# Optimization experiments

Hardware: AMD Instinct MI355X
Metric: run time of the kernel (lower is better)

## Reference

```python
import jax, jax.numpy as jnp
import numpy as np

N = 50000        # nodes
E = 600000       # edges (avg degree 12)
NODE, EDGE, GDIM = 15, 10, 8
HID, L, H = 128, 3, 4
D = HID // H     # per-head dim = 32


def setup_inputs() -> dict:
    key = jax.random.key(0)
    ks = jax.random.split(key, 32)
    f = lambda i, shape, s=0.05: jax.random.normal(ks[i], shape, dtype=jnp.float32) * s
    return {
        "x": f(0, (N, NODE), 1.0),
        "edge_index": jax.random.randint(ks[1], (2, E), 0, N, dtype=jnp.int32),
        "edge_attr": f(2, (E, EDGE), 1.0),
        "u": f(3, (GDIM,), 1.0),
        "enc_w": f(4, (NODE, HID)), "enc_b": f(5, (HID,)),
        "gat_lin_w": f(6, (L, HID, HID)),
        "gat_att_src": f(7, (L, H, D)), "gat_att_dst": f(8, (L, H, D)),
        "gat_lin_edge": f(9, (L, EDGE, HID)), "gat_att_edge": f(10, (L, H, D)),
        "gat_bias": f(11, (L, HID)),
        "ln_g": jnp.ones((L, HID), jnp.float32), "ln_b": jnp.zeros((L, HID), jnp.float32),
        "pool_w": f(12, (3 * HID + GDIM, GDIM)), "pool_b": f(13, (GDIM,)),
        "pool_ln_g": jnp.ones((GDIM,), jnp.float32), "pool_ln_b": jnp.zeros((GDIM,), jnp.float32),
        "head_w1": f(14, (4, HID, 32)), "head_b1": f(15, (4, 32)),
        "head_w2": f(16, (4, 32, 1)), "head_b2": f(17, (4, 1)),
        "strat_w1": f(18, (HID, 32)), "strat_b1": f(19, (32,)),
        "strat_w2": f(20, (32, 5)), "strat_b2": f(21, (5,)),
        "glob_w1": f(22, (GDIM, 32)), "glob_b1": f(23, (32,)),
        "glob_w2": f(24, (32, 4)), "glob_b2": f(25, (4,)),
    }


def _layer_norm(x, g, b, eps=1e-5):
    mu = jnp.mean(x, axis=-1, keepdims=True)
    var = jnp.mean(jnp.square(x - mu), axis=-1, keepdims=True)
    return (x - mu) * jax.lax.rsqrt(var + eps) * g + b


def _forward(edge_index, x, edge_attr, u, enc_w, enc_b, gat_lin_w, gat_att_src,
             gat_att_dst, gat_lin_edge, gat_att_edge, gat_bias, ln_g, ln_b,
             pool_w, pool_b, pool_ln_g, pool_ln_b, head_w1, head_b1, head_w2,
             head_b2, strat_w1, strat_b1, strat_w2, strat_b2, glob_w1, glob_b1,
             glob_w2, glob_b2):
    src0, dst0 = edge_index[0], edge_index[1]
    # PyG GATConv add_self_loops=True with fill_value='mean': self-loop edge
    # attr for node i = mean of edge_attr over edges whose dst is i.
    cnt = jax.ops.segment_sum(jnp.ones((E,), jnp.float32), dst0, num_segments=N)
    ea_self = jax.ops.segment_sum(edge_attr, dst0, num_segments=N) / jnp.maximum(cnt, 1.0)[:, None]
    loop = jnp.arange(N, dtype=src0.dtype)
    src = jnp.concatenate([src0, loop])
    dst = jnp.concatenate([dst0, loop])
    ea = jnp.concatenate([edge_attr, ea_self], axis=0)   # [E+N, EDGE]

    h = jax.nn.relu(x @ enc_w + enc_b)                   # node encoder [N, HID]
    for l in range(L):
        hp = (h @ gat_lin_w[l]).reshape(N, H, D)         # projected nodes
        a_s = jnp.sum(hp * gat_att_src[l], axis=-1)      # [N, H]
        a_d = jnp.sum(hp * gat_att_dst[l], axis=-1)
        ep = (ea @ gat_lin_edge[l]).reshape(-1, H, D)    # [E+N, H, D]
        a_e = jnp.sum(ep * gat_att_edge[l], axis=-1)     # [E+N, H]
        alpha = jax.nn.leaky_relu(a_s[src] + a_d[dst] + a_e, negative_slope=0.2)
        # numerically-stable softmax over incoming edges per dst node
        m = jax.ops.segment_max(alpha, dst, num_segments=N)
        w = jnp.exp(alpha - m[dst])
        denom = jax.ops.segment_sum(w, dst, num_segments=N)
        attn = w / denom[dst]                            # every node has a self-loop
        out = jax.ops.segment_sum(hp[src] * attn[..., None], dst, num_segments=N)
        out = out.reshape(N, HID) + gat_bias[l]
        # residual (shapes match) + dropout(eval=id) + layer norm
        h = _layer_norm(h + out, ln_g[l], ln_b[l])

    pooled = jnp.concatenate([h.mean(0), h.max(0), h.sum(0), u])[None]  # [1, 3*HID+GDIM]
    g = _layer_norm(jax.nn.relu(pooled @ pool_w + pool_b), pool_ln_g, pool_ln_b)

    # four stacked 128->32->1 heads (priority:tanh, coop/urgency/safety:sigmoid)
    z = jax.nn.relu(jnp.einsum('nf,kfh->knh', h, head_w1) + head_b1[:, None, :])
    y = jnp.einsum('knh,kho->kno', z, head_w2) + head_b2[:, None, :]   # [4, N, 1]
    priority = jnp.tanh(y[0])
    cooperation = jax.nn.sigmoid(y[1])
    urgency = jax.nn.sigmoid(y[2])
    safety = jax.nn.sigmoid(y[3])
    strategies = jax.nn.softmax(jax.nn.relu(h @ strat_w1 + strat_b1) @ strat_w2 + strat_b2, axis=-1)
    global_signal = jnp.tanh(jax.nn.relu(g @ glob_w1 + glob_b1) @ glob_w2 + glob_b2)[0]  # [4]
    return (priority, cooperation, urgency, safety, strategies, global_signal)


def reference(x, edge_index, edge_attr, u, enc_w, enc_b, gat_lin_w, gat_att_src,
              gat_att_dst, gat_lin_edge, gat_att_edge, gat_bias, ln_g, ln_b,
              pool_w, pool_b, pool_ln_g, pool_ln_b, head_w1, head_b1, head_w2,
              head_b2, strat_w1, strat_b1, strat_w2, strat_b2, glob_w1, glob_b1,
              glob_w2, glob_b2):
    return _forward(edge_index, x, edge_attr, u, enc_w, enc_b, gat_lin_w,
                    gat_att_src, gat_att_dst, gat_lin_edge, gat_att_edge,
                    gat_bias, ln_g, ln_b, pool_w, pool_b, pool_ln_g, pool_ln_b,
                    head_w1, head_b1, head_w2, head_b2, strat_w1, strat_b1,
                    strat_w2, strat_b2, glob_w1, glob_b1, glob_w2, glob_b2)
```

## Files before the change

kernel.cpp:

```cpp
#include <hip/hip_runtime.h>
#include <hip/hip_bf16.h>
#include <hip/hip_fp16.h>

#define N_NODES 50000
#define N_EDGES 600000
#define TOT_E   (N_EDGES + N_NODES)
#define NLAYER  3
#define PB      200
#define SCB     512
#define NSB     ((N_NODES + SCB - 1)/SCB)
#define CAP     96

typedef __hip_bfloat16 bf16;
__device__ __forceinline__ float b2f(bf16 v){ return __bfloat162float(v); }

__device__ __forceinline__ float ldm(const void* p, long i, int m){
  return m ? ((const float*)p)[i] : b2f(((const bf16*)p)[i]);
}

__global__ void detect_kernel(const void* probe, int* mode){
  __shared__ float red[256];
  int t = threadIdx.x;
  const bf16* p = (const bf16*)probe;
  float mx = 0.f;
  for (int i = t; i < 1920; i += 256){
    float v = fabsf(b2f(p[i]));
    if (!isfinite(v)) v = 1e30f;
    mx = fmaxf(mx, v);
  }
  red[t] = mx; __syncthreads();
  if (t == 0){
    float m = 0.f;
    for (int i = 0; i < 256; i++) m = fmaxf(m, red[i]);
    mode[0] = (m > 1000.0f) ? 1 : 0;
  }
}

__global__ void sentinel_kernel(int host_code, const int* devflags, const int* mode, float* out){
  if (threadIdx.x == 0 && blockIdx.x == 0){
    int code = host_code;
    if (!code && devflags){
      if (devflags[1] > 900)      code = 16384;
      else if (devflags[0])       code = 20480;
    }
    if (code){
      if (mode) code += 512*mode[0];
      out[0] = (float)code;
    }
  }
}

struct CvtTab { const void* s[27]; float* d[27]; int n[27]; };
__global__ void cvt_small_kernel(CvtTab tab, const int* mode){
  int b = blockIdx.x;
  int i = blockIdx.y*256 + threadIdx.x;
  if (i < tab.n[b]) tab.d[b][i] = ldm(tab.s[b], i, mode[0]);
}

__global__ void count_kernel(const int* __restrict__ ei, int* __restrict__ cnt, int* devflags){
  int e = blockIdx.x*256 + threadIdx.x;
  if (e >= N_EDGES) return;
  int s = ei[e], d = ei[N_EDGES + e];
  if (((unsigned)s >= N_NODES) || ((unsigned)d >= N_NODES)) atomicOr(&devflags[0], 1);
  else atomicAdd(&cnt[d], 1);
  if (e < 1024 && ei[2*e + 1] == 0) atomicAdd(&devflags[1], 1);
}

__global__ __launch_bounds__(SCB) void scan1_kernel(const int* __restrict__ cnt, int* __restrict__ bsum){
  __shared__ int ws[SCB/64];
  int i = blockIdx.x*SCB + threadIdx.x;
  int v = (i < N_NODES) ? cnt[i] + 1 : 0;
  int lane = threadIdx.x & 63, w = threadIdx.x >> 6;
  #pragma unroll
  for (int off = 1; off < 64; off <<= 1) v += __shfl_xor(v, off);
  if (lane == 0) ws[w] = v;
  __syncthreads();
  if (threadIdx.x == 0){
    int s = 0;
    #pragma unroll
    for (int k = 0; k < SCB/64; k++) s += ws[k];
    bsum[blockIdx.x] = s;
  }
}

__global__ void scan2_kernel(int* __restrict__ bsum, int* __restrict__ rowptr){
  if (threadIdx.x == 0 && blockIdx.x == 0){
    int run = 0;
    for (int b = 0; b < NSB; b++){ int t = bsum[b]; bsum[b] = run; run += t; }
    rowptr[N_NODES] = run;
  }
}

__global__ __launch_bounds__(SCB) void scan3_kernel(const int* __restrict__ cnt, const int* __restrict__ bsum,
                                                    int* __restrict__ rowptr){
  __shared__ int sm[SCB];
  int t = threadIdx.x;
  int i = blockIdx.x*SCB + t;
  int v = (i < N_NODES) ? cnt[i] + 1 : 0;
  sm[t] = v; __syncthreads();
  for (int off = 1; off < SCB; off <<= 1){
    int add = (t >= off) ? sm[t-off] : 0;
    __syncthreads();
    sm[t] += add;
    __syncthreads();
  }
  if (i < N_NODES) rowptr[i] = bsum[blockIdx.x] + sm[t] - v;
}

__global__ void scatter_kernel(const int* __restrict__ ei, const int* __restrict__ rowptr,
                               int* __restrict__ fill, int* __restrict__ srcs, int* __restrict__ pos_of){
  int e = blockIdx.x*256 + threadIdx.x;
  if (e >= TOT_E) return;
  if (e < N_EDGES){
    int s = ei[e], d = ei[N_EDGES + e];
    int pos = rowptr[d] + atomicAdd(&fill[d], 1);
    srcs[pos] = s; pos_of[e] = pos;
  } else {
    int i = e - N_EDGES;
    srcs[rowptr[i+1] - 1] = i;
  }
}

__global__ void pack_kernel(const float* __restrict__ head_w1, const float* __restrict__ strat_w1,
                            const float* __restrict__ head_b1, const float* __restrict__ strat_b1,
                            float* __restrict__ W1cat, float* __restrict__ b1cat){
  int t = blockIdx.x*256 + threadIdx.x;
  if (t < 128*160){
    int f = t / 160, c = t % 160;
    W1cat[t] = (c < 128) ? head_w1[(c>>5)*4096 + f*32 + (c&31)]
                         : strat_w1[f*32 + (c-128)];
  }
  if (t < 160) b1cat[t] = (t < 128) ? head_b1[t] : strat_b1[t-128];
}

__global__ void mmat_kernel(const float* __restrict__ We, const float* __restrict__ att_edge,
                            float* __restrict__ M){
  int t = threadIdx.x;
  if (t >= 120) return;
  int l = t / 40, r = t % 40, k = r / 4, hh = r % 4;
  float s = 0;
  #pragma unroll
  for (int d = 0; d < 32; d++)
    s += We[l*1280 + k*128 + hh*32 + d] * att_edge[l*128 + hh*32 + d];
  M[t] = s;
}

__global__ __launch_bounds__(128) void encoder_kernel(const void* __restrict__ x_raw, const int* __restrict__ mode,
                                                      const float* __restrict__ enc_w, const float* __restrict__ enc_b,
                                                      float* __restrict__ h){
  __shared__ float xs[16];
  int n = blockIdx.x, j = threadIdx.x;
  if (j < 15) xs[j] = ldm(x_raw, (long)n*15 + j, mode[0]);
  __syncthreads();
  float acc = enc_b[j];
  #pragma unroll
  for (int k = 0; k < 15; k++) acc += xs[k] * enc_w[k*128 + j];
  h[(size_t)n*128 + j] = fmaxf(acc, 0.0f);
}

__global__ void ae_kernel(const void* __restrict__ ea_raw, const int* __restrict__ mode,
                          const float* __restrict__ Mmat, const int* __restrict__ pos_of,
                          float4* __restrict__ aec){
  int e = blockIdx.x*256 + threadIdx.x;
  if (e >= N_EDGES) return;
  int m = mode[0];
  float v[10];
  #pragma unroll
  for (int k = 0; k < 10; k++) v[k] = ldm(ea_raw, (long)e*10 + k, m);
  int p = pos_of[e];
  #pragma unroll
  for (int l = 0; l < 3; l++){
    float r[4];
    #pragma unroll
    for (int hh = 0; hh < 4; hh++){
      float s = 0;
      #pragma unroll
      for (int k = 0; k < 10; k++) s += v[k]*Mmat[l*40 + k*4 + hh];
      r[hh] = s;
    }
    aec[(size_t)l*TOT_E + p] = make_float4(r[0], r[1], r[2], r[3]);
  }
}

#define BK 16
__global__ __launch_bounds__(256) void gemm_kernel(
    const float* __restrict__ A, const float* __restrict__ B, float* __restrict__ Cf,
    __half* __restrict__ Ch, int M, int ldb, int mode, const float* __restrict__ bias,
    const float* __restrict__ att_src, const float* __restrict__ att_dst,
    float* __restrict__ a_s, float* __restrict__ a_d){
  __shared__ float As[BK][128+4];
  __shared__ float Bs[BK][128];
  int t = threadIdx.x;
  int tx = t & 15, ty = t >> 4;
  int n0 = blockIdx.x * 128;
  int j0 = blockIdx.y * 128;
  float acc[8][8];
  #pragma unroll
  for (int i = 0; i < 8; i++)
    #pragma unroll
    for (int j = 0; j < 8; j++) acc[i][j] = 0.0f;

  for (int kb = 0; kb < 128; kb += BK){
    #pragma unroll
    for (int q = 0; q < 2; q++){
      int v = t*2 + q;
      int row = v >> 2, c4 = v & 3;
      int gn = n0 + row;
      float4 f = make_float4(0,0,0,0);
      if (gn < M) f = *(const float4*)(A + (size_t)gn*128 + kb + c4*4);
      As[c4*4+0][row] = f.x; As[c4*4+1][row] = f.y;
      As[c4*4+2][row] = f.z; As[c4*4+3][row] = f.w;
    }
    #pragma unroll
    for (int q = 0; q < 2; q++){
      int v = t*2 + q;
      int kk = v >> 5, j4 = v & 31;
      int gj = j0 + j4*4;
      float4 f = make_float4(0,0,0,0);
      if (gj < ldb) f = *(const float4*)(B + (size_t)(kb+kk)*ldb + gj);
      *(float4*)&Bs[kk][j4*4] = f;
    }
    __syncthreads();
    #pragma unroll
    for (int kk = 0; kk < BK; kk++){
      float4 a0 = *(const float4*)&As[kk][ty*8];
      float4 a1 = *(const float4*)&As[kk][ty*8+4];
      float4 b0 = *(const float4*)&Bs[kk][tx*8];
      float4 b1 = *(const float4*)&Bs[kk][tx*8+4];
      float av[8] = {a0.x,a0.y,a0.z,a0.w,a1.x,a1.y,a1.z,a1.w};
      float bv[8] = {b0.x,b0.y,b0.z,b0.w,b1.x,b1.y,b1.z,b1.w};
      #pragma unroll
      for (int i = 0; i < 8; i++)
        #pragma unroll
        for (int j = 0; j < 8; j++) acc[i][j] += av[i]*bv[j];
    }
    __syncthreads();
  }

  if (mode == 0){
    int head = tx >> 2;
    float as_w[8], ad_w[8];
    #pragma unroll
    for (int jj = 0; jj < 8; jj++){
      int dd = (tx&3)*8 + jj;
      as_w[jj] = att_src[head*32 + dd];
      ad_w[jj] = att_dst[head*32 + dd];
    }
    #pragma unroll
    for (int i = 0; i < 8; i++){
      int gn = n0 + ty*8 + i;
      float ps = 0, pd = 0;
      #pragma unroll
      for (int jj = 0; jj < 8; jj++){ ps += acc[i][jj]*as_w[jj]; pd += acc[i][jj]*ad_w[jj]; }
      ps += __shfl_xor(ps, 1); ps += __shfl_xor(ps, 2);
      pd += __shfl_xor(pd, 1); pd += __shfl_xor(pd, 2);
      if (((tx & 3) == 0) && gn < M){ a_s[gn*4 + head] = ps; a_d[gn*4 + head] = pd; }
      if (gn < M){
        union { __half2 h2[4]; float4 f4; } u;
        #pragma unroll
        for (int q = 0; q < 4; q++){
          __half2 hh;
          hh.x = __float2half(acc[i][2*q]);
          hh.y = __float2half(acc[i][2*q+1]);
          u.h2[q] = hh;
        }
        *(float4*)(Ch + (size_t)gn*128 + tx*8) = u.f4;
      }
    }
  } else {
    int jb = j0 + tx*8;
    bool jok = jb < ldb;
    float bi[8];
    if (jok){
      #pragma unroll
      for (int jj = 0; jj < 8; jj++) bi[jj] = bias[jb+jj];
    }
    #pragma unroll
    for (int i = 0; i < 8; i++){
      int gn = n0 + ty*8 + i;
      if (gn < M && jok){
        float o[8];
        #pragma unroll
        for (int jj = 0; jj < 8; jj++) o[jj] = fmaxf(acc[i][jj] + bi[jj], 0.0f);
        *(float4*)(Cf + (size_t)gn*ldb + jb)     = make_float4(o[0],o[1],o[2],o[3]);
        *(float4*)(Cf + (size_t)gn*ldb + jb + 4) = make_float4(o[4],o[5],o[6],o[7]);
      }
    }
  }
}

__global__ __launch_bounds__(256) void fused_agg_kernel(
    const __half* __restrict__ hp, const float* __restrict__ a_s, const float* __restrict__ a_d,
    const float* __restrict__ aecl, const int* __restrict__ srcs, const int* __restrict__ rowptr,
    const float* __restrict__ bias_l, const float* __restrict__ ln_g_l,
    const float* __restrict__ ln_b_l, float* __restrict__ h){
  __shared__ float wsm[4][CAP*4];
  __shared__ int   ssm[4][CAP];
  int wv = threadIdx.x >> 6;
  int n = blockIdx.x*4 + wv;
  int lane = threadIdx.x & 63;
  int p0 = rowptr[n], p1 = rowptr[n+1];
  int deg = p1 - p0 - 1;
  int hh = lane & 3;
  int esl = lane >> 2;
  float adv = a_d[n*4 + hh];
  float asn = a_s[n*4 + hh];
  bool fits = (deg <= CAP);

  float m = -3.4e38f, ls = 0.f, ssum = 0.f;
  for (int base = 0; base < deg; base += 16){
    int idx = base + esl;
    if (idx < deg){
      int p = p0 + idx;
      float aev = aecl[(size_t)p*4 + hh];
      int sv = srcs[p];
      float al = a_s[sv*4 + hh] + adv + aev;
      al = (al > 0.f) ? al : 0.2f*al;
      ssum += aev;
      if (fits){
        wsm[wv][idx*4 + hh] = al;
        if (hh == 0) ssm[wv][idx] = sv;
      }
      if (al > m){ ls = ls*__expf(m - al) + 1.f; m = al; }
      else ls += __expf(al - m);
    }
  }
  #pragma unroll
  for (int off = 4; off <= 32; off <<= 1){
    float mo = __shfl_xor(m, off);
    float lo = __shfl_xor(ls, off);
    float so = __shfl_xor(ssum, off);
    ssum += so;
    float mn = fmaxf(m, mo);
    ls = ls*__expf(m - mn) + lo*__expf(mo - mn);
    m = mn;
  }
  float aself = ssum / (float)(deg > 0 ? deg : 1);
  float als = asn + adv + aself;
  als = (als > 0.f) ? als : 0.2f*als;
  float mx = fmaxf(m, als);
  float denom = ls*__expf(m - mx) + __expf(als - mx);
  float invd = 1.f/denom;

  if (fits){
    for (int base = 0; base < deg; base += 16){
      int idx = base + esl;
      if (idx < deg){
        float al = wsm[wv][idx*4 + hh];
        wsm[wv][idx*4 + hh] = __expf(al - mx)*invd;
      }
    }
  }

  int hsel = lane >> 4;
  float mxh   = __shfl(mx, hsel);
  float invdh = __shfl(invd, hsel);
  float alsh  = __shfl(als, hsel);

  float acc0 = 0.f, acc1 = 0.f;
  if (fits){
    for (int j = 0; j < deg; j++){
      float w = wsm[wv][j*4 + hsel];
      int  sj = ssm[wv][j];
      __half2 hv = *((const __half2*)(hp + (size_t)sj*128) + lane);
      acc0 += w*__half2float(hv.x);
      acc1 += w*__half2float(hv.y);
    }
  } else {
    for (int base = 0; base < deg; base += 16){
      int idx = base + esl;
      float wgt = 0.f; int sv = 0;
      if (idx < deg){
        int p = p0 + idx;
        float aev = aecl[(size_t)p*4 + hh];
        sv = srcs[p];
        float al = a_s[sv*4 + hh] + adv + aev;
        al = (al > 0.f) ? al : 0.2f*al;
        wgt = __expf(al - mx)*invd;
      }
      int cnt_e = min(16, deg - base);
      for (int j = 0; j < cnt_e; j++){
        float w = __shfl(wgt, j*4 + hsel);
        int  sj = __shfl(sv,  j*4);
        __half2 hv = *((const __half2*)(hp + (size_t)sj*128) + lane);
        acc0 += w*__half2float(hv.x);
        acc1 += w*__half2float(hv.y);
      }
    }
  }
  {
    float w = __expf(alsh - mxh)*invdh;
    __half2 hv = *((const __half2*)(hp + (size_t)n*128) + lane);
    acc0 += w*__half2float(hv.x);
    acc1 += w*__half2float(hv.y);
  }
  float2 res = *(const float2*)(h + (size_t)n*128 + lane*2);
  float2 bi  = *(const float2*)(bias_l + lane*2);
  float v0 = acc0 + bi.x + res.x;
  float v1 = acc1 + bi.y + res.y;
  float s = v0 + v1, sq = v0*v0 + v1*v1;
  #pragma unroll
  for (int off = 32; off >= 1; off >>= 1){ s += __shfl_xor(s, off); sq += __shfl_xor(sq, off); }
  float mu  = s * (1.0f/128.0f);
  float var = sq * (1.0f/128.0f) - mu*mu;
  float rs  = rsqrtf(fmaxf(var, 0.0f) + 1e-5f);
  float2 g  = *(const float2*)(ln_g_l + lane*2);
  float2 bb = *(const float2*)(ln_b_l + lane*2);
  float2 o;
  o.x = (v0 - mu)*rs*g.x + bb.x;
  o.y = (v1 - mu)*rs*g.y + bb.y;
  *(float2*)(h + (size_t)n*128 + lane*2) = o;
}

__global__ __launch_bounds__(128) void pool_part_kernel(const float* __restrict__ h,
                                                        float* __restrict__ psum, float* __restrict__ pmax){
  int b = blockIdx.x, j = threadIdx.x;
  int nb = b*(N_NODES/PB), ne = nb + (N_NODES/PB);
  float s = 0, m = -3.4e38f;
  for (int n = nb; n < ne; n++){ float v = h[(size_t)n*128 + j]; s += v; m = fmaxf(m, v); }
  psum[b*128 + j] = s; pmax[b*128 + j] = m;
}

__global__ __launch_bounds__(128) void global_kernel(
    const float* __restrict__ psum, const float* __restrict__ pmax,
    const float* __restrict__ u, const float* __restrict__ pool_w, const float* __restrict__ pool_b,
    const float* __restrict__ pool_ln_g, const float* __restrict__ pool_ln_b,
    const float* __restrict__ glob_w1, const float* __restrict__ glob_b1,
    const float* __restrict__ glob_w2, const float* __restrict__ glob_b2, float* __restrict__ out_glob){
  __shared__ float pooled[392];
  __shared__ float gv[8];
  __shared__ float t1[32];
  __shared__ float mv[2];
  int t = threadIdx.x;
  float s = 0, m = -3.4e38f;
  for (int b = 0; b < PB; b++){ s += psum[b*128 + t]; m = fmaxf(m, pmax[b*128 + t]); }
  pooled[t]       = s * (1.0f/(float)N_NODES);
  pooled[128 + t] = m;
  pooled[256 + t] = s;
  if (t < 8) pooled[384 + t] = u[t];
  __syncthreads();
  if (t < 8){
    float acc = pool_b[t];
    for (int f = 0; f < 392; f++) acc += pooled[f]*pool_w[f*8 + t];
    gv[t] = fmaxf(acc, 0.0f);
  }
  __syncthreads();
  if (t == 0){
    float mu = 0; for (int i = 0; i < 8; i++) mu += gv[i];
    mu *= 0.125f;
    float var = 0; for (int i = 0; i < 8; i++){ float d = gv[i]-mu; var += d*d; }
    var *= 0.125f;
    mv[0] = mu; mv[1] = rsqrtf(var + 1e-5f);
  }
  __syncthreads();
  float gnorm = (t < 8) ? (gv[t]-mv[0])*mv[1]*pool_ln_g[t] + pool_ln_b[t] : 0.0f;
  __syncthreads();
  if (t < 8) gv[t] = gnorm;
  __syncthreads();
  if (t < 32){
    float acc = glob_b1[t];
    for (int q = 0; q < 8; q++) acc += gv[q]*glob_w1[q*32 + t];
    t1[t] = fmaxf(acc, 0.0f);
  }
  __syncthreads();
  if (t < 4){
    float acc = glob_b2[t];
    for (int mm = 0; mm < 32; mm++) acc += t1[mm]*glob_w2[mm*4 + t];
    out_glob[t] = tanhf(acc);
  }
}

__global__ void finalize_kernel(
    const float* __restrict__ z, const float* __restrict__ head_w2, const float* __restrict__ head_b2,
    const float* __restrict__ strat_w2, const float* __restrict__ strat_b2, float* __restrict__ out){
  int n = blockIdx.x*256 + threadIdx.x;
  if (n >= N_NODES) return;
  const float* zr = z + (size_t)n*160;
  float y[4];
  #pragma unroll
  for (int k = 0; k < 4; k++){
    float acc = head_b2[k];
    #pragma unroll
    for (int m = 0; m < 32; m++) acc += zr[k*32+m]*head_w2[k*32+m];
    y[k] = acc;
  }
  out[n]             = tanhf(y[0]);
  out[N_NODES + n]   = 1.0f/(1.0f + expf(-y[1]));
  out[2*N_NODES + n] = 1.0f/(1.0f + expf(-y[2]));
  out[3*N_NODES + n] = 1.0f/(1.0f + expf(-y[3]));
  float sv[5], mx = -3.4e38f;
  #pragma unroll
  for (int j = 0; j < 5; j++){
    float acc = strat_b2[j];
    #pragma unroll
    for (int m = 0; m < 32; m++) acc += zr[128+m]*strat_w2[m*5+j];
    sv[j] = acc; mx = fmaxf(mx, acc);
  }
  float se = 0;
  #pragma unroll
  for (int j = 0; j < 5; j++){ sv[j] = expf(sv[j]-mx); se += sv[j]; }
  float inv = 1.0f/se;
  #pragma unroll
  for (int j = 0; j < 5; j++) out[4*N_NODES + (size_t)n*5 + j] = sv[j]*inv;
}

extern "C" void kernel_launch(void* const* d_in, const int* in_sizes, int n_in,
                              void* d_out, int out_size, void* d_ws, size_t ws_size,
                              hipStream_t stream){
  float* out = (float*)d_out;

  static const int exp_sizes[30] = {
    750000, 1200000, 6000000, 8, 1920, 128, 49152, 384, 384, 3840, 384,
    384, 384, 384, 3136, 8, 8, 8, 16384, 128, 128, 4, 4096, 32, 160, 5,
    256, 32, 128, 4 };
  int host_code = 0;
  if (n_in != 30){
    int nn = n_in < 0 ? 0 : (n_in > 63 ? 63 : n_in);
    host_code = 4096 + 32*nn;
  } else {
    for (int i = 0; i < 30; i++)
      if (in_sizes[i] != exp_sizes[i]){ host_code = 1024 + 8*i; break; }
  }
  if (!host_code && out_size != 9*N_NODES + 4) host_code = 12288;
  if (host_code){
    sentinel_kernel<<<1, 64, 0, stream>>>(host_code, nullptr, nullptr, out);
    return;
  }

  const int* ei = (const int*)d_in[1];

  char* wsp = (char*)d_ws;
  size_t off = 0;
  auto alloc = [&](size_t bytes)->char*{ char* p = wsp + off; off += (bytes + 255) & ~(size_t)255; return p; };

  float*  h    = (float*)alloc((size_t)N_NODES*128*4);
  __half* hp   = (__half*)alloc((size_t)N_NODES*128*2);
  float*  a_s  = (float*)alloc((size_t)N_NODES*4*4);
  float*  a_d  = (float*)alloc((size_t)N_NODES*4*4);
  float*  aec  = (float*)alloc((size_t)3*TOT_E*16);
  float*  zbuf = (float*)hp;
  int*   srcs   = (int*)alloc((size_t)TOT_E*4);
  int*   pos_of = (int*)alloc((size_t)N_EDGES*4);
  int*   rowptr = (int*)alloc((size_t)(N_NODES+1)*4);
  int*   bsum   = (int*)alloc((size_t)NSB*4);

  const int SN = 27;
  static const int sn_sizes[SN] = {
    8, 1920, 128, 49152, 384, 384, 3840, 384, 384, 384, 384,
    3136, 8, 8, 8, 16384, 128, 128, 4, 4096, 32, 160, 5, 256, 32, 128, 4 };
  static const int sn_input[SN] = {
    3, 4, 5, 6, 7, 8, 9, 10, 11, 12, 13, 14, 15, 16, 17,
    18, 19, 20, 21, 22, 23, 24, 25, 26, 27, 28, 29 };
  float* sarr[SN];
  for (int i = 0; i < SN; i++) sarr[i] = (float*)alloc((size_t)sn_sizes[i]*4);
  float* u_c       = sarr[0];
  float* enc_w_c   = sarr[1];
  float* enc_b_c   = sarr[2];
  float* Wl        = sarr[3];
  float* att_src_c = sarr[4];
  float* att_dst_c = sarr[5];
  float* lin_e_c   = sarr[6];
  float* att_e_c   = sarr[7];
  float* bias_c    = sarr[8];
  float* ln_g_c    = sarr[9];
  float* ln_b_c    = sarr[10];
  float* pool_w_c  = sarr[11];
  float* pool_b_c  = sarr[12];
  float* pln_g_c   = sarr[13];
  float* pln_b_c   = sarr[14];
  float* head_w1_c = sarr[15];
  float* head_b1_c = sarr[16];
  float* head_w2_c = sarr[17];
  float* head_b2_c = sarr[18];
  float* strat_w1_c= sarr[19];
  float* strat_b1_c= sarr[20];
  float* strat_w2_c= sarr[21];
  float* strat_b2_c= sarr[22];
  float* glob_w1_c = sarr[23];
  float* glob_b1_c = sarr[24];
  float* glob_w2_c = sarr[25];
  float* glob_b2_c = sarr[26];

  float* W1cat  = (float*)alloc((size_t)128*160*4);
  float* b1cat  = (float*)alloc(160*4);
  float* Mmat   = (float*)alloc(3*40*4);
  int*   mode   = (int*)alloc(256);
  float* psum   = (float*)alloc((size_t)PB*128*4);
  float* pmax   = (float*)alloc((size_t)PB*128*4);
  size_t zero_begin = off;
  int*   devflags = (int*)alloc(256);
  int*   cnt      = (int*)alloc((size_t)N_NODES*4);
  int*   fill     = (int*)alloc((size_t)N_NODES*4);
  size_t zero_bytes = off - zero_begin;

  if (ws_size < off){
    sentinel_kernel<<<1, 64, 0, stream>>>(8192, nullptr, nullptr, out);
    return;
  }

  hipMemsetAsync(wsp + zero_begin, 0, zero_bytes, stream);

  detect_kernel<<<1, 256, 0, stream>>>(d_in[4], mode);

  CvtTab tab;
  for (int i = 0; i < SN; i++){ tab.s[i] = d_in[sn_input[i]]; tab.d[i] = sarr[i]; tab.n[i] = sn_sizes[i]; }
  cvt_small_kernel<<<dim3(SN, 192), 256, 0, stream>>>(tab, mode);

  pack_kernel<<<(128*160 + 255)/256, 256, 0, stream>>>(head_w1_c, strat_w1_c, head_b1_c, strat_b1_c, W1cat, b1cat);
  mmat_kernel<<<1, 128, 0, stream>>>(lin_e_c, att_e_c, Mmat);
  count_kernel<<<(N_EDGES + 255)/256, 256, 0, stream>>>(ei, cnt, devflags);
  scan1_kernel<<<NSB, SCB, 0, stream>>>(cnt, bsum);
  scan2_kernel<<<1, 64, 0, stream>>>(bsum, rowptr);
  scan3_kernel<<<NSB, SCB, 0, stream>>>(cnt, bsum, rowptr);
  scatter_kernel<<<(TOT_E + 255)/256, 256, 0, stream>>>(ei, rowptr, fill, srcs, pos_of);
  ae_kernel<<<(N_EDGES + 255)/256, 256, 0, stream>>>(d_in[2], mode, Mmat, pos_of, (float4*)aec);
  encoder_kernel<<<N_NODES, 128, 0, stream>>>(d_in[0], mode, enc_w_c, enc_b_c, h);

  const int gx = (N_NODES + 127)/128;
  for (int l = 0; l < NLAYER; l++){
    gemm_kernel<<<dim3(gx, 1), 256, 0, stream>>>(h, Wl + (size_t)l*128*128, nullptr, hp, N_NODES, 128, 0,
                                                 nullptr, att_src_c + l*128, att_dst_c + l*128, a_s, a_d);
    fused_agg_kernel<<<N_NODES/4, 256, 0, stream>>>(hp, a_s, a_d, aec + (size_t)l*TOT_E*4, srcs, rowptr,
                                                    bias_c + l*128, ln_g_c + l*128, ln_b_c + l*128, h);
  }

  pool_part_kernel<<<PB, 128, 0, stream>>>(h, psum, pmax);
  global_kernel<<<1, 128, 0, stream>>>(psum, pmax, u_c, pool_w_c, pool_b_c, pln_g_c, pln_b_c,
                                       glob_w1_c, glob_b1_c, glob_w2_c, glob_b2_c, out + 9*N_NODES);
  gemm_kernel<<<dim3(gx, 2), 256, 0, stream>>>(h, W1cat, zbuf, nullptr, N_NODES, 160, 1, b1cat,
                                               nullptr, nullptr, nullptr, nullptr);
  finalize_kernel<<<(N_NODES + 255)/256, 256, 0, stream>>>(zbuf, head_w2_c, head_b2_c, strat_w2_c, strat_b2_c, out);
  sentinel_kernel<<<1, 64, 0, stream>>>(0, devflags, mode, out);
}
```

Before: 554.8 us.

## Replace FP32 SIMT GEMMs with split-bf16 MFMA GEMMs and fold attention projections

Swaps the shared-memory FP32 tiled GEMM for an MFMA kernel that emulates FP32 precision with three bf16 products (hi*hi, lo*hi, hi*lo). B matrices are pre-split into hi/lo bf16 and packed in MFMA fragment order by new setup kernels. The attention src/dst dot products are folded into extra weight columns (W·att), so a_s and a_d come out of the same GEMM as the projected features. This adds MFMA work and some precision loss from the dropped lo*lo term. The output stores also become scalar and strided rather than vectorized.

```diff
diff --git a/kernel.cpp b/kernel.cpp
--- a/kernel.cpp
+++ b/kernel.cpp
@@ -12,10 +12,18 @@
 #define CAP     96
 
 typedef __hip_bfloat16 bf16;
+typedef __attribute__((ext_vector_type(8))) short short8;
+typedef __attribute__((ext_vector_type(4))) float floatx4;
+
 __device__ __forceinline__ float b2f(bf16 v){ return __bfloat162float(v); }
 
 __device__ __forceinline__ float ldm(const void* p, long i, int m){
   return m ? ((const float*)p)[i] : b2f(((const bf16*)p)[i]);
+}
+
+__device__ __forceinline__ unsigned bfr(float f){
+  unsigned u = __float_as_uint(f);
+  return (u + 0x7fffu + ((u>>16)&1u)) >> 16;
 }
 
 __global__ void detect_kernel(const void* probe, int* mode){
@@ -145,6 +153,54 @@
   M[t] = s;
 }
 
+__global__ void vsd_kernel(const float* __restrict__ Wl, const float* __restrict__ att_src,
+                           const float* __restrict__ att_dst, float* __restrict__ vsd){
+  int t = blockIdx.x*256 + threadIdx.x;
+  if (t >= 3*128*8) return;
+  int l = t >> 10, r = t & 1023;
+  int k = r >> 3, c = r & 7;
+  int sd = c >> 2, hh = c & 3;
+  const float* w = Wl + l*16384 + k*128 + hh*32;
+  const float* a = (sd ? att_dst : att_src) + l*128 + hh*32;
+  float s = 0;
+  #pragma unroll
+  for (int d = 0; d < 32; d++) s += w[d]*a[d];
+  vsd[t] = s;
+}
+
+__global__ void pack_bsw_kernel(const float* __restrict__ Wl, const float* __restrict__ vsd,
+                                const float* __restrict__ W1cat,
+                                ushort* __restrict__ Bsw0, ushort* __restrict__ Bsw1){
+  int tid = blockIdx.x*256 + threadIdx.x;
+  if (tid < 3*4*144*32){
+    int l = tid / 18432, rr = tid % 18432;
+    int kt = rr / 4608, r2 = rr % 4608;
+    int n = r2 / 32, kk = r2 & 31;
+    int k = kt*32 + kk;
+    float f;
+    if (n < 128)      f = Wl[l*16384 + k*128 + n];
+    else if (n < 136) f = vsd[l*1024 + k*8 + (n - 128)];
+    else              f = 0.f;
+    unsigned hb = bfr(f);
+    float fh = __uint_as_float(hb<<16);
+    unsigned lb = bfr(f - fh);
+    Bsw0[(size_t)(l*2+0)*18432 + kt*4608 + n*32 + kk] = (ushort)hb;
+    Bsw0[(size_t)(l*2+1)*18432 + kt*4608 + n*32 + kk] = (ushort)lb;
+  } else {
+    int t2 = tid - 3*4*144*32;
+    if (t2 >= 4*160*32) return;
+    int kt = t2 / 5120, r2 = t2 % 5120;
+    int n = r2 / 32, kk = r2 & 31;
+    int k = kt*32 + kk;
+    float f = W1cat[k*160 + n];
+    unsigned hb = bfr(f);
+    float fh = __uint_as_float(hb<<16);
+    unsigned lb = bfr(f - fh);
+    Bsw1[kt*5120 + n*32 + kk]          = (ushort)hb;
+    Bsw1[4*5120 + kt*5120 + n*32 + kk] = (ushort)lb;
+  }
+}
+
 __global__ __launch_bounds__(128) void encoder_kernel(const void* __restrict__ x_raw, const int* __restrict__ mode,
                                                       const float* __restrict__ enc_w, const float* __restrict__ enc_b,
                                                       float* __restrict__ h){
@@ -182,108 +238,59 @@
   }
 }
 
-#define BK 16
-__global__ __launch_bounds__(256) void gemm_kernel(
-    const float* __restrict__ A, const float* __restrict__ B, float* __restrict__ Cf,
-    __half* __restrict__ Ch, int M, int ldb, int mode, const float* __restrict__ bias,
-    const float* __restrict__ att_src, const float* __restrict__ att_dst,
+template<int NT, int MODE>
+__global__ __launch_bounds__(256) void gemm_mfma(
+    const float* __restrict__ A, const ushort* __restrict__ Bhi, const ushort* __restrict__ Blo,
+    int M, const float* __restrict__ bias, __half* __restrict__ Ch, float* __restrict__ Cf,
     float* __restrict__ a_s, float* __restrict__ a_d){
-  __shared__ float As[BK][128+4];
-  __shared__ float Bs[BK][128];
-  int t = threadIdx.x;
-  int tx = t & 15, ty = t >> 4;
-  int n0 = blockIdx.x * 128;
-  int j0 = blockIdx.y * 128;
-  float acc[8][8];
-  #pragma unroll
-  for (int i = 0; i < 8; i++)
+  int wv = threadIdx.x >> 6, lane = threadIdx.x & 63;
+  int nl = lane & 15, q = lane >> 4;
+  int row0 = blockIdx.x*64 + wv*16;
+  if (row0 >= M) return;
+  floatx4 acc[NT];
+  #pragma unroll
+  for (int t = 0; t < NT; t++) acc[t] = (floatx4){0.f, 0.f, 0.f, 0.f};
+  int ra = row0 + nl; if (ra > M-1) ra = M-1;
+  const float* arow = A + (size_t)ra*128 + q*8;
+  #pragma unroll
+  for (int kt = 0; kt < 4; kt++){
+    float4 a0 = *(const float4*)(arow + kt*32);
+    float4 a1 = *(const float4*)(arow + kt*32 + 4);
+    float af[8] = {a0.x,a0.y,a0.z,a0.w,a1.x,a1.y,a1.z,a1.w};
+    short8 ahi, alo;
     #pragma unroll
-    for (int j = 0; j < 8; j++) acc[i][j] = 0.0f;
-
-  for (int kb = 0; kb < 128; kb += BK){
+    for (int j = 0; j < 8; j++){
+      unsigned hb = bfr(af[j]);
+      float fh = __uint_as_float(hb<<16);
+      unsigned lb = bfr(af[j] - fh);
+      ahi[j] = (short)hb; alo[j] = (short)lb;
+    }
+    const ushort* bh = Bhi + kt*(NT*16*32) + nl*32 + q*8;
+    const ushort* bl = Blo + kt*(NT*16*32) + nl*32 + q*8;
     #pragma unroll
-    for (int q = 0; q < 2; q++){
-      int v = t*2 + q;
-      int row = v >> 2, c4 = v & 3;
-      int gn = n0 + row;
-      float4 f = make_float4(0,0,0,0);
-      if (gn < M) f = *(const float4*)(A + (size_t)gn*128 + kb + c4*4);
-      As[c4*4+0][row] = f.x; As[c4*4+1][row] = f.y;
-      As[c4*4+2][row] = f.z; As[c4*4+3][row] = f.w;
-    }
-    #pragma unroll
-    for (int q = 0; q < 2; q++){
-      int v = t*2 + q;
-      int kk = v >> 5, j4 = v & 31;
-      int gj = j0 + j4*4;
-      float4 f = make_float4(0,0,0,0);
-      if (gj < ldb) f = *(const float4*)(B + (size_t)(kb+kk)*ldb + gj);
-      *(float4*)&Bs[kk][j4*4] = f;
-    }
-    __syncthreads();
-    #pragma unroll
-    for (int kk = 0; kk < BK; kk++){
-      float4 a0 = *(const float4*)&As[kk][ty*8];
-      float4 a1 = *(const float4*)&As[kk][ty*8+4];
-      float4 b0 = *(const float4*)&Bs[kk][tx*8];
-      float4 b1 = *(const float4*)&Bs[kk][tx*8+4];
-      float av[8] = {a0.x,a0.y,a0.z,a0.w,a1.x,a1.y,a1.z,a1.w};
-      float bv[8] = {b0.x,b0.y,b0.z,b0.w,b1.x,b1.y,b1.z,b1.w};
+    for (int t = 0; t < NT; t++){
+      short8 b0 = *(const short8*)(bh + t*512);
+      short8 b1 = *(const short8*)(bl + t*512);
+      acc[t] = __builtin_amdgcn_mfma_f32_16x16x32_bf16(ahi, b0, acc[t], 0, 0, 0);
+      acc[t] = __builtin_amdgcn_mfma_f32_16x16x32_bf16(alo, b0, acc[t], 0, 0, 0);
+      acc[t] = __builtin_amdgcn_mfma_f32_16x16x32_bf16(ahi, b1, acc[t], 0, 0, 0);
+    }
+  }
+  #pragma unroll
+  for (int r = 0; r < 4; r++){
+    int row = row0 + q*4 + r;
+    if (row >= M) continue;
+    if (MODE == 0){
       #pragma unroll
-      for (int i = 0; i < 8; i++)
-        #pragma unroll
-        for (int j = 0; j < 8; j++) acc[i][j] += av[i]*bv[j];
-    }
-    __syncthreads();
-  }
-
-  if (mode == 0){
-    int head = tx >> 2;
-    float as_w[8], ad_w[8];
-    #pragma unroll
-    for (int jj = 0; jj < 8; jj++){
-      int dd = (tx&3)*8 + jj;
-      as_w[jj] = att_src[head*32 + dd];
-      ad_w[jj] = att_dst[head*32 + dd];
-    }
-    #pragma unroll
-    for (int i = 0; i < 8; i++){
-      int gn = n0 + ty*8 + i;
-      float ps = 0, pd = 0;
+      for (int t = 0; t < 8; t++)
+        Ch[(size_t)row*128 + t*16 + nl] = __float2half(acc[t][r]);
+      if (nl < 4)      a_s[row*4 + nl]       = acc[8][r];
+      else if (nl < 8) a_d[row*4 + (nl - 4)] = acc[8][r];
+    } else {
       #pragma unroll
-      for (int jj = 0; jj < 8; jj++){ ps += acc[i][jj]*as_w[jj]; pd += acc[i][jj]*ad_w[jj]; }
-      ps += __shfl_xor(ps, 1); ps += __shfl_xor(ps, 2);
-      pd += __shfl_xor(pd, 1); pd += __shfl_xor(pd, 2);
-      if (((tx & 3) == 0) && gn < M){ a_s[gn*4 + head] = ps; a_d[gn*4 + head] = pd; }
-      if (gn < M){
-        union { __half2 h2[4]; float4 f4; } u;
-        #pragma unroll
-        for (int q = 0; q < 4; q++){
-          __half2 hh;
-          hh.x = __float2half(acc[i][2*q]);
-          hh.y = __float2half(acc[i][2*q+1]);
-          u.h2[q] = hh;
-        }
-        *(float4*)(Ch + (size_t)gn*128 + tx*8) = u.f4;
-      }
-    }
-  } else {
-    int jb = j0 + tx*8;
-    bool jok = jb < ldb;
-    float bi[8];
-    if (jok){
-      #pragma unroll
-      for (int jj = 0; jj < 8; jj++) bi[jj] = bias[jb+jj];
-    }
-    #pragma unroll
-    for (int i = 0; i < 8; i++){
-      int gn = n0 + ty*8 + i;
-      if (gn < M && jok){
-        float o[8];
-        #pragma unroll
-        for (int jj = 0; jj < 8; jj++) o[jj] = fmaxf(acc[i][jj] + bi[jj], 0.0f);
-        *(float4*)(Cf + (size_t)gn*ldb + jb)     = make_float4(o[0],o[1],o[2],o[3]);
-        *(float4*)(Cf + (size_t)gn*ldb + jb + 4) = make_float4(o[4],o[5],o[6],o[7]);
+      for (int t = 0; t < NT; t++){
+        int col = t*16 + nl;
+        Cf[(size_t)row*160 + col] = fmaxf(acc[t][r] + bias[col], 0.f);
       }
     }
   }
@@ -581,12 +588,15 @@
   float* glob_w2_c = sarr[25];
   float* glob_b2_c = sarr[26];
 
-  float* W1cat  = (float*)alloc((size_t)128*160*4);
-  float* b1cat  = (float*)alloc(160*4);
-  float* Mmat   = (float*)alloc(3*40*4);
-  int*   mode   = (int*)alloc(256);
-  float* psum   = (float*)alloc((size_t)PB*128*4);
-  float* pmax   = (float*)alloc((size_t)PB*128*4);
+  float*  W1cat = (float*)alloc((size_t)128*160*4);
+  float*  b1cat = (float*)alloc(160*4);
+  float*  Mmat  = (float*)alloc(3*40*4);
+  float*  vsd   = (float*)alloc((size_t)3*128*8*4);
+  ushort* Bsw0  = (ushort*)alloc((size_t)3*2*4*144*32*2);
+  ushort* Bsw1  = (ushort*)alloc((size_t)2*4*160*32*2);
+  int*    mode  = (int*)alloc(256);
+  float*  psum  = (float*)alloc((size_t)PB*128*4);
+  float*  pmax  = (float*)alloc((size_t)PB*128*4);
   size_t zero_begin = off;
   int*   devflags = (int*)alloc(256);
   int*   cnt      = (int*)alloc((size_t)N_NODES*4);
@@ -608,6 +618,9 @@
 
   pack_kernel<<<(128*160 + 255)/256, 256, 0, stream>>>(head_w1_c, strat_w1_c, head_b1_c, strat_b1_c, W1cat, b1cat);
   mmat_kernel<<<1, 128, 0, stream>>>(lin_e_c, att_e_c, Mmat);
+  vsd_kernel<<<(3*128*8 + 255)/256, 256, 0, stream>>>(Wl, att_src_c, att_dst_c, vsd);
+  pack_bsw_kernel<<<(3*4*144*32 + 4*160*32 + 255)/256, 256, 0, stream>>>(Wl, vsd, W1cat, Bsw0, Bsw1);
+
   count_kernel<<<(N_EDGES + 255)/256, 256, 0, stream>>>(ei, cnt, devflags);
   scan1_kernel<<<NSB, SCB, 0, stream>>>(cnt, bsum);
   scan2_kernel<<<1, 64, 0, stream>>>(bsum, rowptr);
@@ -616,10 +629,11 @@
   ae_kernel<<<(N_EDGES + 255)/256, 256, 0, stream>>>(d_in[2], mode, Mmat, pos_of, (float4*)aec);
   encoder_kernel<<<N_NODES, 128, 0, stream>>>(d_in[0], mode, enc_w_c, enc_b_c, h);
 
-  const int gx = (N_NODES + 127)/128;
+  const int gb = (N_NODES + 63)/64;
   for (int l = 0; l < NLAYER; l++){
-    gemm_kernel<<<dim3(gx, 1), 256, 0, stream>>>(h, Wl + (size_t)l*128*128, nullptr, hp, N_NODES, 128, 0,
-                                                 nullptr, att_src_c + l*128, att_dst_c + l*128, a_s, a_d);
+    const ushort* Bhi = Bsw0 + (size_t)l*2*18432;
+    const ushort* Blo = Bhi + 18432;
+    gemm_mfma<9,0><<<gb, 256, 0, stream>>>(h, Bhi, Blo, N_NODES, nullptr, hp, nullptr, a_s, a_d);
     fused_agg_kernel<<<N_NODES/4, 256, 0, stream>>>(hp, a_s, a_d, aec + (size_t)l*TOT_E*4, srcs, rowptr,
                                                     bias_c + l*128, ln_g_c + l*128, ln_b_c + l*128, h);
   }
@@ -627,8 +641,8 @@
   pool_part_kernel<<<PB, 128, 0, stream>>>(h, psum, pmax);
   global_kernel<<<1, 128, 0, stream>>>(psum, pmax, u_c, pool_w_c, pool_b_c, pln_g_c, pln_b_c,
                                        glob_w1_c, glob_b1_c, glob_w2_c, glob_b2_c, out + 9*N_NODES);
-  gemm_kernel<<<dim3(gx, 2), 256, 0, stream>>>(h, W1cat, zbuf, nullptr, N_NODES, 160, 1, b1cat,
-                                               nullptr, nullptr, nullptr, nullptr);
+  gemm_mfma<10,1><<<gb, 256, 0, stream>>>(h, Bsw1, Bsw1 + 4*5120, N_NODES, b1cat, nullptr, zbuf,
+                                          nullptr, nullptr);
   finalize_kernel<<<(N_NODES + 255)/256, 256, 0, stream>>>(zbuf, head_w2_c, head_b2_c, strat_w2_c, strat_b2_c, out);
   sentinel_kernel<<<1, 64, 0, stream>>>(0, devflags, mode, out);
 }
```

New measurement: 531.0 us. 4.3% less time.
